# Kernel optimization log

Measured on AMD Instinct MI355X. Metric: run time of the kernel, lower is better.

Reference implementation:

```python
import jax, jax.numpy as jnp
import numpy as np

B, S, D = 2, 2048, 2048
H, KVH = 32, 8
HD = D // H          # 64
N_REP = H // KVH     # 4
NEG = -1e9


def setup_inputs() -> dict:
    key = jax.random.key(0)
    ks = jax.random.split(key, 5)
    x = jax.random.normal(ks[0], (B, S, D), dtype=jnp.float32)
    std = 0.02
    wq = jax.random.normal(ks[1], (H * HD, D), dtype=jnp.float32) * std
    wk = jax.random.normal(ks[2], (KVH * HD, D), dtype=jnp.float32) * std
    wv = jax.random.normal(ks[3], (KVH * HD, D), dtype=jnp.float32) * std
    wo = jax.random.normal(ks[4], (D, H * HD), dtype=jnp.float32) * std
    # RoPE tables: (S, HD//2)
    inv_freq = 1.0 / (10000.0 ** (np.arange(0, HD, 2, dtype=np.float32) / HD))
    t = np.arange(S, dtype=np.float32)
    freqs = np.outer(t, inv_freq)
    freqs_cos = jnp.asarray(np.cos(freqs))
    freqs_sin = jnp.asarray(np.sin(freqs))
    # additive causal mask [1,1,S,S]
    causal = np.tril(np.ones((S, S), dtype=bool))
    mask = jnp.asarray(np.where(causal, 0.0, NEG).astype(np.float32))[None, None]
    return {"x": x, "wq": wq, "wk": wk, "wv": wv, "wo": wo,
            "freqs_cos": freqs_cos, "freqs_sin": freqs_sin, "mask": mask}


def _apply_rope(t, cos, sin):
    # t: [B,S,nh,HD]; cos/sin: [S, HD//2]
    tr = t.reshape(t.shape[:-1] + (HD // 2, 2))
    r, i = tr[..., 0], tr[..., 1]
    c = cos[None, :, None, :]
    s = sin[None, :, None, :]
    out_r = r * c - i * s
    out_i = r * s + i * c
    return jnp.stack([out_r, out_i], axis=-1).reshape(t.shape)


def reference(x, wq, wk, wv, wo, freqs_cos, freqs_sin, mask):
    b, s, _ = x.shape
    q = (x @ wq.T).reshape(b, s, H, HD)
    k = (x @ wk.T).reshape(b, s, KVH, HD)
    v = (x @ wv.T).reshape(b, s, KVH, HD)
    q = _apply_rope(q, freqs_cos, freqs_sin)
    k = _apply_rope(k, freqs_cos, freqs_sin)
    # repeat_kv (GQA expansion) then move heads forward: [B,H,S,HD]
    k = jnp.repeat(k, N_REP, axis=2)
    v = jnp.repeat(v, N_REP, axis=2)
    q = q.transpose(0, 2, 1, 3)
    k = k.transpose(0, 2, 1, 3)
    v = v.transpose(0, 2, 1, 3)
    scale = 1.0 / jnp.sqrt(jnp.float32(HD))
    scores = jnp.einsum("bhqd,bhkd->bhqk", q, k) * scale + mask[:, :, :s, :s]
    attn = jax.nn.softmax(scores, axis=-1)
    out = jnp.einsum("bhqk,bhkd->bhqd", attn, v)
    out = out.transpose(0, 2, 1, 3).reshape(b, s, H * HD)
    return out @ wo.T
```

## Files before the change

kernel.cpp:

```cpp
#include <hip/hip_runtime.h>
#include <hip/hip_bf16.h>
#include <stdint.h>


#define NEG_BIG (-1e9f)
#define SCALE_LOG2 0.18033688011112042f
#define DEFER_THR 10.0f

typedef __bf16 bf16x8 __attribute__((ext_vector_type(8)));
typedef float f32x4 __attribute__((ext_vector_type(4)));
typedef float f32x16 __attribute__((ext_vector_type(16)));
typedef uint16_t u16x8 __attribute__((ext_vector_type(8)));
typedef uint32_t u32x4 __attribute__((ext_vector_type(4)));

__device__ inline uint16_t f2bf(float x) {
    __hip_bfloat16 h = __float2bfloat16(x);
    return __builtin_bit_cast(uint16_t, h);
}
__device__ inline float bf2f(uint16_t u) {
    uint32_t t = (uint32_t)u << 16;
    return __builtin_bit_cast(float, t);
}

__device__ inline void async_cp16(const void* g, void* l) {
    __builtin_amdgcn_global_load_lds(
        (const __attribute__((address_space(1))) uint32_t*)g,
        (__attribute__((address_space(3))) uint32_t*)l,
        16 , 0 , 0 );
}

__global__ void cvt4(const float* __restrict__ in, uint16_t* __restrict__ out, int n4) {
    int i = blockIdx.x * blockDim.x + threadIdx.x;
    if (i >= n4) return;
    const float4 v = ((const float4*)in)[i];
    ushort4 o;
    o.x = f2bf(v.x); o.y = f2bf(v.y); o.z = f2bf(v.z); o.w = f2bf(v.w);
    ((ushort4*)out)[i] = o;
}

__global__ void build_wqkv(const float* __restrict__ wq, const float* __restrict__ wk,
                           const float* __restrict__ wv, uint16_t* __restrict__ out) {
    int i = blockIdx.x * blockDim.x + threadIdx.x;
    if (i >= (3072 * 2048) / 4) return;
    int e = i * 4;
    int row = e >> 11;
    int col = e & 2047;
    const float* src = (row < 2048) ? (wq + (long)row * 2048 + col)
                     : (row < 2560) ? (wk + (long)(row - 2048) * 2048 + col)
                                    : (wv + (long)(row - 2560) * 2048 + col);
    const float4 v = *(const float4*)src;
    ushort4 o;
    o.x = f2bf(v.x); o.y = f2bf(v.y); o.z = f2bf(v.z); o.w = f2bf(v.w);
    ((ushort4*)(out + e))[0] = o;
}

template <int BN, int OUT_BF16>
__global__ __launch_bounds__(512) void gemm256(const uint16_t* __restrict__ A,
                                               const uint16_t* __restrict__ Bw,
                                               void* __restrict__ Cout,
                                               int M, int N, int K) {
    constexpr int WN = BN / 4;
    constexpr int NF = WN / 16;
    constexpr int BROUNDS = BN / 64;

    __shared__ __align__(16) uint16_t As[2][256 * 64];
    __shared__ __align__(16) uint16_t Bs[2][BN * 64];

    const int tid = threadIdx.x;
    const int l = tid & 63;
    const int w = tid >> 6;
    const int wmi = w >> 2;
    const int wni = w & 3;
    const int c = l & 15, g = l >> 4;
    const long row0 = (long)blockIdx.x * 256;
    const long col0 = (long)blockIdx.y * BN;

    f32x4 acc[8][NF] = {};

    auto STAGE = [&](int buf, int t) {
        const long k0 = (long)t * 64;
#pragma unroll
        for (int rr = 0; rr < 4; ++rr) {
            const int e = rr * 512 + tid;
            const int r = e >> 3;
            const int gs = (e & 7) ^ (r & 7);
            async_cp16(A + (row0 + r) * (long)K + k0 + gs * 8, &As[buf][e * 8]);
        }
#pragma unroll
        for (int rr = 0; rr < BROUNDS; ++rr) {
            const int e = rr * 512 + tid;
            const int r = e >> 3;
            const int gs = (e & 7) ^ (r & 7);
            async_cp16(Bw + (col0 + r) * (long)K + k0 + gs * 8, &Bs[buf][e * 8]);
        }
    };

    STAGE(0, 0);
    __syncthreads();

    const int nt = K / 64;
    for (int t = 0; t < nt; ++t) {
        const int cur = t & 1;
        if (t + 1 < nt) STAGE(cur ^ 1, t + 1);

#pragma unroll
        for (int kk = 0; kk < 2; ++kk) {
            bf16x8 bF[NF];
#pragma unroll
            for (int n = 0; n < NF; ++n) {
                const int rb = wni * WN + n * 16 + c;
                const int sp = ((kk * 4 + g) ^ (c & 7));
                bF[n] = *(const bf16x8*)&Bs[cur][rb * 64 + sp * 8];
            }
#pragma unroll
            for (int mh = 0; mh < 2; ++mh) {
                bf16x8 aF[4];
#pragma unroll
                for (int mm = 0; mm < 4; ++mm) {
                    const int ra = wmi * 128 + (mh * 4 + mm) * 16 + c;
                    const int sp = ((kk * 4 + g) ^ (c & 7));
                    aF[mm] = *(const bf16x8*)&As[cur][ra * 64 + sp * 8];
                }
                __builtin_amdgcn_s_setprio(1);
#pragma unroll
                for (int mm = 0; mm < 4; ++mm)
#pragma unroll
                    for (int n = 0; n < NF; ++n)
                        acc[mh * 4 + mm][n] = __builtin_amdgcn_mfma_f32_16x16x32_bf16(
                            aF[mm], bF[n], acc[mh * 4 + mm][n], 0, 0, 0);
                __builtin_amdgcn_s_setprio(0);
            }
        }
        if (t + 1 < nt) __syncthreads();
    }

#pragma unroll
    for (int m = 0; m < 8; ++m) {
        const long rg = row0 + wmi * 128 + m * 16 + g * 4;
#pragma unroll
        for (int n = 0; n < NF; ++n) {
            const long cg = col0 + wni * WN + n * 16 + c;
#pragma unroll
            for (int r = 0; r < 4; ++r) {
                float v = acc[m][n][r];
                if (OUT_BF16)
                    ((uint16_t*)Cout)[(rg + r) * (long)N + cg] = f2bf(v);
                else
                    ((float*)Cout)[(rg + r) * (long)N + cg] = v;
            }
        }
    }
}

__global__ void rope_q(uint16_t* __restrict__ qkv,
                       const float* __restrict__ cosT,
                       const float* __restrict__ sinT) {
    int idx = blockIdx.x * blockDim.x + threadIdx.x;
    if (idx >= 4096 * 1024) return;
    int m = idx >> 10;
    int j = idx & 1023;
    int s = m & 2047;
    int d2 = j & 31;
    float cc = cosT[s * 32 + d2];
    float ss = sinT[s * 32 + d2];
    uint32_t* p = (uint32_t*)(qkv + (long)m * 3072 + 2 * j);
    uint32_t v = *p;
    float re = bf2f((uint16_t)(v & 0xffffu));
    float im = bf2f((uint16_t)(v >> 16));
    float orr = (re * cc - im * ss) * SCALE_LOG2;
    float oi  = (re * ss + im * cc) * SCALE_LOG2;
    *p = (uint32_t)f2bf(orr) | ((uint32_t)f2bf(oi) << 16);
}

__global__ void pack_kv(const uint16_t* __restrict__ qkv,
                        const float* __restrict__ cosT,
                        const float* __restrict__ sinT,
                        uint16_t* __restrict__ Kpk,
                        uint16_t* __restrict__ Vpk) {
    const int gw = (blockIdx.x * blockDim.x + threadIdx.x) >> 6;
    const int l = threadIdx.x & 63;
    const int lq = l & 31, hi = l >> 5;
    if (gw < 4096) {
        const int wid = gw;
        const int s = wid & 3;
        const int tile = (wid >> 2) & 63;
        const int bk = wid >> 8;
        const int b = bk >> 3, kvh = bk & 7;
        const int key = 32 * tile + lq;
        const uint16_t* src = qkv + (long)(b * 2048 + key) * 3072
                            + 2048 + kvh * 64 + 16 * s + 8 * hi;
        u16x8 v = *(const u16x8*)src;
        const int d2b = 8 * s + 4 * hi;
        u16x8 o;
#pragma unroll
        for (int p = 0; p < 4; ++p) {
            const float cc = cosT[key * 32 + d2b + p];
            const float ss = sinT[key * 32 + d2b + p];
            const float re = bf2f(v[2 * p]);
            const float im = bf2f(v[2 * p + 1]);
            o[2 * p]     = f2bf(re * cc - im * ss);
            o[2 * p + 1] = f2bf(re * ss + im * cc);
        }
        *(u16x8*)(Kpk + (((long)(bk * 64 + tile) * 4 + s) * 64 + l) * 8) = o;
    } else {
        const int wid = gw - 4096;
        const int s2 = wid & 1;
        const int nd = (wid >> 1) & 1;
        const int tile = (wid >> 2) & 63;
        const int bk = wid >> 8;
        const int b = bk >> 3, kvh = bk & 7;
        const int key0 = 32 * tile + 16 * s2 + 8 * hi;
        const uint16_t* src = qkv + (long)(b * 2048 + key0) * 3072
                            + 2560 + kvh * 64 + nd * 32 + lq;
        u16x8 v;
#pragma unroll
        for (int jj = 0; jj < 8; ++jj) v[jj] = src[(long)jj * 3072];
        *(u16x8*)(Vpk + ((((long)(bk * 64 + tile) * 2 + nd) * 2 + s2) * 64 + l) * 8) = v;
    }
}

__device__ inline void pack_pf(const float pr[16], bf16x8 pf[2]) {
    uint32_t wds[8];
#pragma unroll
    for (int m = 0; m < 8; ++m)
        wds[m] = (uint32_t)f2bf(pr[2 * m]) | ((uint32_t)f2bf(pr[2 * m + 1]) << 16);
    asm volatile("v_permlane32_swap_b32 %0, %1" : "+v"(wds[0]), "+v"(wds[2]));
    asm volatile("v_permlane32_swap_b32 %0, %1" : "+v"(wds[1]), "+v"(wds[3]));
    asm volatile("v_permlane32_swap_b32 %0, %1" : "+v"(wds[4]), "+v"(wds[6]));
    asm volatile("v_permlane32_swap_b32 %0, %1" : "+v"(wds[5]), "+v"(wds[7]));
    u32x4 pk0 = {wds[0], wds[1], wds[2], wds[3]};
    u32x4 pk1 = {wds[4], wds[5], wds[6], wds[7]};
    pf[0] = __builtin_bit_cast(bf16x8, pk0);
    pf[1] = __builtin_bit_cast(bf16x8, pk1);
}

__global__ __launch_bounds__(128, 4) void attn_fwd(const uint16_t* __restrict__ qkv,
                                                   const uint16_t* __restrict__ Kpk,
                                                   const uint16_t* __restrict__ Vpk,
                                                   uint16_t* __restrict__ outb) {
    const int bid = blockIdx.x;
    const int gh = bid & 63;
    const int j = 63 - (bid >> 6);
    const int t0 = threadIdx.x;
    const int l = t0 & 63, ww = t0 >> 6;
    const int b = gh >> 5, h = gh & 31;
    const int kvh = h >> 2;
    const int bk = b * 8 + kvh;
    const int lq = l & 31, hi = l >> 5;
    const int q = 32 * j + lq;

    __shared__ float smM[64], smL[64];
    __shared__ float smO[64][33];

    const uint16_t* qrow = qkv + (long)(b * 2048 + q) * 3072 + h * 64 + 8 * hi;
    bf16x8 qf[4];
#pragma unroll
    for (int s = 0; s < 4; ++s) qf[s] = *(const bf16x8*)(qrow + 16 * s);

    float m_run = -1e30f, l_run = 0.f;
    f32x16 accO[2] = {};

    const uint16_t* kbase = Kpk + (long)bk * 64 * 2048 + (long)l * 8;
    const uint16_t* vbase = Vpk + (long)bk * 64 * 2048 + (long)l * 8;
    const int nT = (j + 2) >> 1;
    const int h0 = nT >> 1;
    const int tbeg = ww ? h0 : 0;
    const int tend = ww ? nT : h0;

    for (int t = tbeg; t < tend; ++t) {
        bf16x8 kf[2][4];
#pragma unroll
        for (int u = 0; u < 2; ++u)
#pragma unroll
            for (int s = 0; s < 4; ++s)
                kf[u][s] = *(const bf16x8*)(kbase + (long)(2 * t + u) * 2048 + s * 512);

        f32x16 st0 = {}, st1 = {};
        __builtin_amdgcn_s_setprio(1);
#pragma unroll
        for (int s = 0; s < 4; ++s)
            st0 = __builtin_amdgcn_mfma_f32_32x32x16_bf16(kf[0][s], qf[s], st0, 0, 0, 0);
#pragma unroll
        for (int s = 0; s < 4; ++s)
            st1 = __builtin_amdgcn_mfma_f32_32x32x16_bf16(kf[1][s], qf[s], st1, 0, 0, 0);
        __builtin_amdgcn_s_setprio(0);

        bf16x8 vf[2][2][2];
#pragma unroll
        for (int u = 0; u < 2; ++u)
#pragma unroll
            for (int nd = 0; nd < 2; ++nd)
#pragma unroll
                for (int s2 = 0; s2 < 2; ++s2)
                    vf[u][nd][s2] = *(const bf16x8*)(vbase + (long)(2 * t + u) * 2048 + nd * 1024 + s2 * 512);

        if (t == nT - 1) {
            const int tq0 = lq + ((j - 2 * t) << 5) - 4 * hi;
            const int tq1 = tq0 - 32;
#pragma unroll
            for (int r = 0; r < 16; ++r) {
                const int kc = (r & 3) + 8 * (r >> 2);
                if (kc > tq0) st0[r] = NEG_BIG;
                if (kc > tq1) st1[r] = NEG_BIG;
            }
        }

        float mx[16];
#pragma unroll
        for (int r = 0; r < 16; ++r) mx[r] = fmaxf(st0[r], st1[r]);
#pragma unroll
        for (int off = 8; off; off >>= 1)
#pragma unroll
            for (int r = 0; r < 8; ++r)
                if (r < off) mx[r] = fmaxf(mx[r], mx[r + off]);
        const float vm = fmaxf(mx[0], __shfl_xor(mx[0], 32));

        if (!__all(vm - m_run <= DEFER_THR)) {
            const float mnew = fmaxf(m_run, vm);
            const float alpha = __builtin_amdgcn_exp2f(m_run - mnew);
            m_run = mnew;
            l_run *= alpha;
#pragma unroll
            for (int nd = 0; nd < 2; ++nd)
#pragma unroll
                for (int r = 0; r < 16; ++r) accO[nd][r] *= alpha;
        }

        float pr0[16], pr1[16], sm[8];
#pragma unroll
        for (int r = 0; r < 16; ++r) pr0[r] = __builtin_amdgcn_exp2f(st0[r] - m_run);
#pragma unroll
        for (int r = 0; r < 16; ++r) pr1[r] = __builtin_amdgcn_exp2f(st1[r] - m_run);
#pragma unroll
        for (int m = 0; m < 8; ++m)
            sm[m] = (pr0[2 * m] + pr0[2 * m + 1]) + (pr1[2 * m] + pr1[2 * m + 1]);
#pragma unroll
        for (int off = 4; off; off >>= 1)
#pragma unroll
            for (int r = 0; r < 4; ++r)
                if (r < off) sm[r] += sm[r + off];
        l_run += sm[0] + __shfl_xor(sm[0], 32);

        bf16x8 pf0[2], pf1[2];
        pack_pf(pr0, pf0);
        pack_pf(pr1, pf1);

        __builtin_amdgcn_s_setprio(1);
#pragma unroll
        for (int nd = 0; nd < 2; ++nd) {
            accO[nd] = __builtin_amdgcn_mfma_f32_32x32x16_bf16(vf[0][nd][0], pf0[0], accO[nd], 0, 0, 0);
            accO[nd] = __builtin_amdgcn_mfma_f32_32x32x16_bf16(vf[0][nd][1], pf0[1], accO[nd], 0, 0, 0);
            accO[nd] = __builtin_amdgcn_mfma_f32_32x32x16_bf16(vf[1][nd][0], pf1[0], accO[nd], 0, 0, 0);
            accO[nd] = __builtin_amdgcn_mfma_f32_32x32x16_bf16(vf[1][nd][1], pf1[1], accO[nd], 0, 0, 0);
        }
        __builtin_amdgcn_s_setprio(0);
    }

    if (ww == 0) {
        smM[l] = m_run;
        smL[l] = l_run;
#pragma unroll
        for (int nd = 0; nd < 2; ++nd)
#pragma unroll
            for (int r = 0; r < 16; ++r) smO[l][nd * 16 + r] = accO[nd][r];
    }
    __syncthreads();
    if (ww == 1) {
        const float m0 = smM[l], l0 = smL[l];
        const float mf = fmaxf(m0, m_run);
        const float a0 = __builtin_amdgcn_exp2f(m0 - mf);
        const float a1 = __builtin_amdgcn_exp2f(m_run - mf);
        const float lf = l0 * a0 + l_run * a1;
        const float invl = 1.0f / lf;
        uint16_t* orow = outb + (long)(b * 2048 + q) * 2048 + h * 64 + 4 * hi;
#pragma unroll
        for (int nd = 0; nd < 2; ++nd)
#pragma unroll
            for (int m = 0; m < 4; ++m) {
                ushort4 o;
#pragma unroll
                for (int r4 = 0; r4 < 4; ++r4) {
                    const int r = 4 * m + r4;
                    const float vmerged = smO[l][nd * 16 + r] * a0 + accO[nd][r] * a1;
                    ((uint16_t*)&o)[r4] = f2bf(vmerged * invl);
                }
                *(ushort4*)(orow + nd * 32 + 8 * m) = o;
            }
    }
}

extern "C" void kernel_launch(void* const* d_in, const int* in_sizes, int n_in,
                              void* d_out, int out_size, void* d_ws, size_t ws_size,
                              hipStream_t stream) {
    const float* x    = (const float*)d_in[0];
    const float* wq   = (const float*)d_in[1];
    const float* wk   = (const float*)d_in[2];
    const float* wv   = (const float*)d_in[3];
    const float* wo   = (const float*)d_in[4];
    const float* fcos = (const float*)d_in[5];
    const float* fsin = (const float*)d_in[6];
    float* out = (float*)d_out;

    uint8_t* ws = (uint8_t*)d_ws;
    const size_t MiB = 1048576;
    uint16_t* x_bf   = (uint16_t*)(ws);
    uint16_t* w_bf   = (uint16_t*)(ws + 16 * MiB);
    uint16_t* qkv_bf = (uint16_t*)(ws + 28 * MiB);
    uint16_t* att_bf = x_bf;
    uint16_t* Kpk    = (uint16_t*)(ws + 16 * MiB);
    uint16_t* Vpk    = (uint16_t*)(ws + 20 * MiB);
    uint16_t* wo_bf  = (uint16_t*)(ws + 16 * MiB);

    cvt4<<<(2097152 + 255) / 256, 256, 0, stream>>>(x, x_bf, 2097152);
    build_wqkv<<<(1572864 + 255) / 256, 256, 0, stream>>>(wq, wk, wv, w_bf);

    gemm256<192, 1><<<dim3(16, 16), 512, 0, stream>>>(x_bf, w_bf, qkv_bf, 4096, 3072, 2048);

    rope_q<<<16384, 256, 0, stream>>>(qkv_bf, fcos, fsin);
    pack_kv<<<2048, 256, 0, stream>>>(qkv_bf, fcos, fsin, Kpk, Vpk);

    attn_fwd<<<4096, 128, 0, stream>>>(qkv_bf, Kpk, Vpk, att_bf);

    cvt4<<<(1048576 + 255) / 256, 256, 0, stream>>>(wo, wo_bf, 1048576);
    gemm256<128, 0><<<dim3(16, 16), 512, 0, stream>>>(att_bf, wo_bf, out, 4096, 2048, 2048);
}
```

Measured before the change: 212.7 us.

## Share K/V tiles across four query-row waves via double-buffered LDS staging

```diff
diff --git a/kernel.cpp b/kernel.cpp
--- a/kernel.cpp
+++ b/kernel.cpp
@@ -234,23 +234,27 @@
     pf[1] = __builtin_bit_cast(bf16x8, pk1);
 }
 
-__global__ __launch_bounds__(128, 4) void attn_fwd(const uint16_t* __restrict__ qkv,
-                                                   const uint16_t* __restrict__ Kpk,
-                                                   const uint16_t* __restrict__ Vpk,
-                                                   uint16_t* __restrict__ outb) {
+__global__ __launch_bounds__(256) void attn_fwd(const uint16_t* __restrict__ qkv,
+                                                const uint16_t* __restrict__ Kpk,
+                                                const uint16_t* __restrict__ Vpk,
+                                                uint16_t* __restrict__ outb) {
     const int bid = blockIdx.x;
     const int gh = bid & 63;
-    const int j = 63 - (bid >> 6);
-    const int t0 = threadIdx.x;
-    const int l = t0 & 63, ww = t0 >> 6;
+    const int p = bid >> 6;
+    const int a = p & 3, bs = p >> 2;
+    const int j2 = (bs == 0) ? (15 - a) : (bs == 1) ? (8 + a)
+                 : (bs == 2) ? (4 + a) : (3 - a);
+    const int tid = threadIdx.x;
+    const int l = tid & 63, ww = tid >> 6;
     const int b = gh >> 5, h = gh & 31;
     const int kvh = h >> 2;
     const int bk = b * 8 + kvh;
     const int lq = l & 31, hi = l >> 5;
-    const int q = 32 * j + lq;
-
-    __shared__ float smM[64], smL[64];
-    __shared__ float smO[64][33];
+    const int rs = 4 * j2 + ww;
+    const int q = 32 * rs + lq;
+
+    __shared__ __align__(16) uint16_t Ks[2][4096];
+    __shared__ __align__(16) uint16_t Vs[2][4096];
 
     const uint16_t* qrow = qkv + (long)(b * 2048 + q) * 3072 + h * 64 + 8 * hi;
     bf16x8 qf[4];
@@ -260,133 +264,133 @@
     float m_run = -1e30f, l_run = 0.f;
     f32x16 accO[2] = {};
 
-    const uint16_t* kbase = Kpk + (long)bk * 64 * 2048 + (long)l * 8;
-    const uint16_t* vbase = Vpk + (long)bk * 64 * 2048 + (long)l * 8;
-    const int nT = (j + 2) >> 1;
-    const int h0 = nT >> 1;
-    const int tbeg = ww ? h0 : 0;
-    const int tend = ww ? nT : h0;
-
-    for (int t = tbeg; t < tend; ++t) {
-        bf16x8 kf[2][4];
-#pragma unroll
-        for (int u = 0; u < 2; ++u)
+    const int nT_blk = 2 * j2 + 2;
+    const int nT_w = (rs >> 1) + 1;
+
+    const uint16_t* kvbase = Kpk + (long)bk * 64 * 2048;
+    const uint16_t* vvbase = Vpk + (long)bk * 64 * 2048;
+
+    auto STAGE = [&](int buf, int t) {
+        const uint16_t* ks = kvbase + (long)(2 * t) * 2048 + tid * 8;
+        const uint16_t* vs = vvbase + (long)(2 * t) * 2048 + tid * 8;
+        async_cp16(ks,        &Ks[buf][tid * 8]);
+        async_cp16(ks + 2048, &Ks[buf][2048 + tid * 8]);
+        async_cp16(vs,        &Vs[buf][tid * 8]);
+        async_cp16(vs + 2048, &Vs[buf][2048 + tid * 8]);
+    };
+
+    STAGE(0, 0);
+    __syncthreads();
+
+    for (int t = 0; t < nT_blk; ++t) {
+        const int cur = t & 1;
+        if (t + 1 < nT_blk) STAGE(cur ^ 1, t + 1);
+
+        if (t < nT_w) {
+            bf16x8 kf[2][4];
+#pragma unroll
+            for (int u = 0; u < 2; ++u)
+#pragma unroll
+                for (int s = 0; s < 4; ++s)
+                    kf[u][s] = *(const bf16x8*)&Ks[cur][u * 2048 + s * 512 + l * 8];
+
+            f32x16 st0 = {}, st1 = {};
+            __builtin_amdgcn_s_setprio(1);
 #pragma unroll
             for (int s = 0; s < 4; ++s)
-                kf[u][s] = *(const bf16x8*)(kbase + (long)(2 * t + u) * 2048 + s * 512);
-
-        f32x16 st0 = {}, st1 = {};
-        __builtin_amdgcn_s_setprio(1);
-#pragma unroll
-        for (int s = 0; s < 4; ++s)
-            st0 = __builtin_amdgcn_mfma_f32_32x32x16_bf16(kf[0][s], qf[s], st0, 0, 0, 0);
-#pragma unroll
-        for (int s = 0; s < 4; ++s)
-            st1 = __builtin_amdgcn_mfma_f32_32x32x16_bf16(kf[1][s], qf[s], st1, 0, 0, 0);
-        __builtin_amdgcn_s_setprio(0);
-
-        bf16x8 vf[2][2][2];
-#pragma unroll
-        for (int u = 0; u < 2; ++u)
-#pragma unroll
-            for (int nd = 0; nd < 2; ++nd)
-#pragma unroll
-                for (int s2 = 0; s2 < 2; ++s2)
-                    vf[u][nd][s2] = *(const bf16x8*)(vbase + (long)(2 * t + u) * 2048 + nd * 1024 + s2 * 512);
-
-        if (t == nT - 1) {
-            const int tq0 = lq + ((j - 2 * t) << 5) - 4 * hi;
-            const int tq1 = tq0 - 32;
-#pragma unroll
-            for (int r = 0; r < 16; ++r) {
-                const int kc = (r & 3) + 8 * (r >> 2);
-                if (kc > tq0) st0[r] = NEG_BIG;
-                if (kc > tq1) st1[r] = NEG_BIG;
-            }
-        }
-
-        float mx[16];
-#pragma unroll
-        for (int r = 0; r < 16; ++r) mx[r] = fmaxf(st0[r], st1[r]);
-#pragma unroll
-        for (int off = 8; off; off >>= 1)
-#pragma unroll
-            for (int r = 0; r < 8; ++r)
-                if (r < off) mx[r] = fmaxf(mx[r], mx[r + off]);
-        const float vm = fmaxf(mx[0], __shfl_xor(mx[0], 32));
-
-        if (!__all(vm - m_run <= DEFER_THR)) {
-            const float mnew = fmaxf(m_run, vm);
-            const float alpha = __builtin_amdgcn_exp2f(m_run - mnew);
-            m_run = mnew;
-            l_run *= alpha;
-#pragma unroll
-            for (int nd = 0; nd < 2; ++nd)
-#pragma unroll
-                for (int r = 0; r < 16; ++r) accO[nd][r] *= alpha;
-        }
-
-        float pr0[16], pr1[16], sm[8];
-#pragma unroll
-        for (int r = 0; r < 16; ++r) pr0[r] = __builtin_amdgcn_exp2f(st0[r] - m_run);
-#pragma unroll
-        for (int r = 0; r < 16; ++r) pr1[r] = __builtin_amdgcn_exp2f(st1[r] - m_run);
-#pragma unroll
-        for (int m = 0; m < 8; ++m)
-            sm[m] = (pr0[2 * m] + pr0[2 * m + 1]) + (pr1[2 * m] + pr1[2 * m + 1]);
-#pragma unroll
-        for (int off = 4; off; off >>= 1)
-#pragma unroll
-            for (int r = 0; r < 4; ++r)
-                if (r < off) sm[r] += sm[r + off];
-        l_run += sm[0] + __shfl_xor(sm[0], 32);
-
-        bf16x8 pf0[2], pf1[2];
-        pack_pf(pr0, pf0);
-        pack_pf(pr1, pf1);
-
-        __builtin_amdgcn_s_setprio(1);
-#pragma unroll
-        for (int nd = 0; nd < 2; ++nd) {
-            accO[nd] = __builtin_amdgcn_mfma_f32_32x32x16_bf16(vf[0][nd][0], pf0[0], accO[nd], 0, 0, 0);
-            accO[nd] = __builtin_amdgcn_mfma_f32_32x32x16_bf16(vf[0][nd][1], pf0[1], accO[nd], 0, 0, 0);
-            accO[nd] = __builtin_amdgcn_mfma_f32_32x32x16_bf16(vf[1][nd][0], pf1[0], accO[nd], 0, 0, 0);
-            accO[nd] = __builtin_amdgcn_mfma_f32_32x32x16_bf16(vf[1][nd][1], pf1[1], accO[nd], 0, 0, 0);
-        }
-        __builtin_amdgcn_s_setprio(0);
+                st0 = __builtin_amdgcn_mfma_f32_32x32x16_bf16(kf[0][s], qf[s], st0, 0, 0, 0);
+#pragma unroll
+            for (int s = 0; s < 4; ++s)
+                st1 = __builtin_amdgcn_mfma_f32_32x32x16_bf16(kf[1][s], qf[s], st1, 0, 0, 0);
+            __builtin_amdgcn_s_setprio(0);
+
+            bf16x8 vf[2][2][2];
+#pragma unroll
+            for (int u = 0; u < 2; ++u)
+#pragma unroll
+                for (int nd = 0; nd < 2; ++nd)
+#pragma unroll
+                    for (int s2 = 0; s2 < 2; ++s2)
+                        vf[u][nd][s2] = *(const bf16x8*)&Vs[cur][u * 2048 + nd * 1024 + s2 * 512 + l * 8];
+
+            if (t == nT_w - 1) {
+                const int tq0 = 32 * rs + lq - 64 * t - 4 * hi;
+                const int tq1 = tq0 - 32;
+#pragma unroll
+                for (int r = 0; r < 16; ++r) {
+                    const int kc = (r & 3) + 8 * (r >> 2);
+                    if (kc > tq0) st0[r] = NEG_BIG;
+                    if (kc > tq1) st1[r] = NEG_BIG;
+                }
+            }
+
+            float mx[16];
+#pragma unroll
+            for (int r = 0; r < 16; ++r) mx[r] = fmaxf(st0[r], st1[r]);
+#pragma unroll
+            for (int off = 8; off; off >>= 1)
+#pragma unroll
+                for (int r = 0; r < 8; ++r)
+                    if (r < off) mx[r] = fmaxf(mx[r], mx[r + off]);
+            const float vm = fmaxf(mx[0], __shfl_xor(mx[0], 32));
+
+            if (!__all(vm - m_run <= DEFER_THR)) {
+                const float mnew = fmaxf(m_run, vm);
+                const float alpha = __builtin_amdgcn_exp2f(m_run - mnew);
+                m_run = mnew;
+                l_run *= alpha;
+#pragma unroll
+                for (int nd = 0; nd < 2; ++nd)
+#pragma unroll
+                    for (int r = 0; r < 16; ++r) accO[nd][r] *= alpha;
+            }
+
+            float pr0[16], pr1[16], sm[8];
+#pragma unroll
+            for (int r = 0; r < 16; ++r) pr0[r] = __builtin_amdgcn_exp2f(st0[r] - m_run);
+#pragma unroll
+            for (int r = 0; r < 16; ++r) pr1[r] = __builtin_amdgcn_exp2f(st1[r] - m_run);
+#pragma unroll
+            for (int m = 0; m < 8; ++m)
+                sm[m] = (pr0[2 * m] + pr0[2 * m + 1]) + (pr1[2 * m] + pr1[2 * m + 1]);
+#pragma unroll
+            for (int off = 4; off; off >>= 1)
+#pragma unroll
+                for (int r = 0; r < 4; ++r)
+                    if (r < off) sm[r] += sm[r + off];
+            l_run += sm[0] + __shfl_xor(sm[0], 32);
+
+            bf16x8 pf0[2], pf1[2];
+            pack_pf(pr0, pf0);
+            pack_pf(pr1, pf1);
+
+            __builtin_amdgcn_s_setprio(1);
+#pragma unroll
+            for (int nd = 0; nd < 2; ++nd) {
+                accO[nd] = __builtin_amdgcn_mfma_f32_32x32x16_bf16(vf[0][nd][0], pf0[0], accO[nd], 0, 0, 0);
+                accO[nd] = __builtin_amdgcn_mfma_f32_32x32x16_bf16(vf[0][nd][1], pf0[1], accO[nd], 0, 0, 0);
+                accO[nd] = __builtin_amdgcn_mfma_f32_32x32x16_bf16(vf[1][nd][0], pf1[0], accO[nd], 0, 0, 0);
+                accO[nd] = __builtin_amdgcn_mfma_f32_32x32x16_bf16(vf[1][nd][1], pf1[1], accO[nd], 0, 0, 0);
+            }
+            __builtin_amdgcn_s_setprio(0);
+        }
+
+        __syncthreads();
     }
 
-    if (ww == 0) {
-        smM[l] = m_run;
-        smL[l] = l_run;
-#pragma unroll
-        for (int nd = 0; nd < 2; ++nd)
-#pragma unroll
-            for (int r = 0; r < 16; ++r) smO[l][nd * 16 + r] = accO[nd][r];
-    }
-    __syncthreads();
-    if (ww == 1) {
-        const float m0 = smM[l], l0 = smL[l];
-        const float mf = fmaxf(m0, m_run);
-        const float a0 = __builtin_amdgcn_exp2f(m0 - mf);
-        const float a1 = __builtin_amdgcn_exp2f(m_run - mf);
-        const float lf = l0 * a0 + l_run * a1;
-        const float invl = 1.0f / lf;
-        uint16_t* orow = outb + (long)(b * 2048 + q) * 2048 + h * 64 + 4 * hi;
-#pragma unroll
-        for (int nd = 0; nd < 2; ++nd)
-#pragma unroll
-            for (int m = 0; m < 4; ++m) {
-                ushort4 o;
-#pragma unroll
-                for (int r4 = 0; r4 < 4; ++r4) {
-                    const int r = 4 * m + r4;
-                    const float vmerged = smO[l][nd * 16 + r] * a0 + accO[nd][r] * a1;
-                    ((uint16_t*)&o)[r4] = f2bf(vmerged * invl);
-                }
-                *(ushort4*)(orow + nd * 32 + 8 * m) = o;
-            }
-    }
+    const float invl = 1.0f / l_run;
+    uint16_t* orow = outb + (long)(b * 2048 + q) * 2048 + h * 64 + 4 * hi;
+#pragma unroll
+    for (int nd = 0; nd < 2; ++nd)
+#pragma unroll
+        for (int m = 0; m < 4; ++m) {
+            ushort4 o;
+            o.x = f2bf(accO[nd][4 * m + 0] * invl);
+            o.y = f2bf(accO[nd][4 * m + 1] * invl);
+            o.z = f2bf(accO[nd][4 * m + 2] * invl);
+            o.w = f2bf(accO[nd][4 * m + 3] * invl);
+            *(ushort4*)(orow + nd * 32 + 8 * m) = o;
+        }
 }
 
 extern "C" void kernel_launch(void* const* d_in, const int* in_sizes, int n_in,
@@ -419,7 +423,7 @@
     rope_q<<<16384, 256, 0, stream>>>(qkv_bf, fcos, fsin);
     pack_kv<<<2048, 256, 0, stream>>>(qkv_bf, fcos, fsin, Kpk, Vpk);
 
-    attn_fwd<<<4096, 128, 0, stream>>>(qkv_bf, Kpk, Vpk, att_bf);
+    attn_fwd<<<1024, 256, 0, stream>>>(qkv_bf, Kpk, Vpk, att_bf);
 
     cvt4<<<(1048576 + 255) / 256, 256, 0, stream>>>(wo, wo_bf, 1048576);
     gemm256<128, 0><<<dim3(16, 16), 512, 0, stream>>>(att_bf, wo_bf, out, 4096, 2048, 2048);
```

After: 224.0 us. 5.3% more time.
